# Kernel tuning notes

Measured on AMD Instinct MI355X. Metric: run time of the kernel, lower is better.

Reference implementation:

```python
import jax, jax.numpy as jnp
import numpy as np

# Layered-DAG regularization of the dynamic active_path graph.
H, N, BATCH, D, R = 6, 16, 32, 512, 64   # hop levels, nodes/level, batch, dim, low-rank
M = (H - 1) * N                           # nodes with weights (levels 1..H-1)
ETA_W = 0.015
LAM_C, LAM_R = 0.65, 0.35
THETA0 = 0.5
SPEC_MIN, SPEC_MAX = 0.3, 4.0
BETA1, BETA2, EPS = 0.9, 0.999, 1e-8
W_MAX = float(np.sqrt(D) * 2.0)
DW_CLIP = 5.0


def _spectral_norm(A1, B1):
    # largest singular value of W = A1 @ B1.T via power iteration using only low-rank products
    d = A1.shape[0]
    def body(_, u):
        w = A1 @ (B1.T @ (B1 @ (A1.T @ u)))  # (W W^T) u
        return w / (jnp.linalg.norm(w) + 1e-12)
    u0 = jnp.ones((d,), A1.dtype) / jnp.sqrt(jnp.asarray(d, A1.dtype))
    u = jax.lax.fori_loop(0, 20, body, u0)
    return jnp.linalg.norm(B1 @ (A1.T @ u))


def _update_node(A1, B1, mA, vA, mB, vB, Vin, T_local):
    # dual-signal (contrastive + retrograde) weight update, Adam step t=1, is_positive=True
    W = A1 @ B1.T                       # (D, D)
    Vw = Vin @ W.T                      # (BATCH, D) pre-activation (record.V_weighted)
    Vout = jnp.tanh(Vw)                 # record.V_out (tanh primitive)
    fprime = 1.0 - Vout ** 2            # primitive_derivative for tanh
    goodness = (Vout ** 2).sum(-1).mean()
    theta = THETA0 * ((Vin ** 2).sum(-1).mean() + 1e-9)   # goodness_scale_input=True
    delta = goodness - theta
    Vout_grad = (Vout * fprime * delta).mean(0)
    Vin_mean = Vin.mean(0)
    dW_c = jnp.outer(Vout_grad, Vin_mean)
    dW_r = jnp.outer(T_local.mean(0) * fprime.mean(0), Vin_mean)
    dW = LAM_C * dW_c + LAM_R * dW_r
    gnorm = jnp.linalg.norm(dW)
    dW = dW * jnp.where(gnorm > DW_CLIP, DW_CLIP / (gnorm + 1e-12), 1.0)
    gA = dW @ B1
    gB = dW.T @ A1
    mA_n = BETA1 * mA + (1 - BETA1) * gA
    vA_n = BETA2 * vA + (1 - BETA2) * gA ** 2
    A_new = A1 - ETA_W * (mA_n / (1 - BETA1)) / (jnp.sqrt(vA_n / (1 - BETA2)) + EPS)
    mB_n = BETA1 * mB + (1 - BETA1) * gB
    vB_n = BETA2 * vB + (1 - BETA2) * gB ** 2
    B_new = B1 - ETA_W * (mB_n / (1 - BETA1)) / (jnp.sqrt(vB_n / (1 - BETA2)) + EPS)
    return jnp.clip(A_new, -W_MAX, W_MAX), jnp.clip(B_new, -W_MAX, W_MAX)


def _forward(Y_hat, Y_star, V_edges, A, Bw, m_A, v_A, m_B, v_B):
    T_v = (Y_star - Y_hat) / jnp.sqrt(jnp.asarray(D, Y_hat.dtype))
    mse = jnp.mean((Y_star - Y_hat) ** 2)

    # proportional blame: per-edge mean-over-batch L2 norm of the contribution
    norms = jnp.linalg.norm(V_edges, axis=-1).mean(-1)           # (H-1, Ndst, Nsrc)
    w_blame = norms / (norms.sum(-1, keepdims=True) + 1e-9)

    spec = jax.vmap(jax.vmap(_spectral_norm))(A, Bw)             # (H-1, N)
    scale = jax.lax.stop_gradient(jnp.clip(spec, SPEC_MIN, SPEC_MAX))  # torch.tensor() detaches

    # retrograde flow in reverse topological (hop) order; output node = (level H-1, node 0)
    T_top = jnp.zeros((N, BATCH, D), Y_hat.dtype).at[0].set(T_v)

    def step(T_curr, xs):
        w_h, s_h = xs                                            # (Ndst,Nsrc), (Ndst,)
        tnorm = jnp.linalg.norm(T_curr, axis=-1).mean(-1)        # (Ndst,)
        edge_t = s_h[:, None] * w_h * tnorm[:, None]             # ||T_upstream|| per edge
        T_prev = jnp.einsum('j,ji,jbd->ibd', s_h, w_h, T_curr)   # blame-weighted scatter
        return T_prev, (T_prev, edge_t)

    _, (Ts, edge_t) = jax.lax.scan(step, T_top, (w_blame[::-1], scale[::-1]))
    T_all = jnp.concatenate([Ts[::-1], T_top[None]], axis=0)     # (H, N, BATCH, D), by level
    edge_tensions = edge_t[::-1]                                 # (H-1, Ndst, Nsrc)

    V_in = V_edges.sum(axis=2)                                   # inbox sum -> (H-1, N, BATCH, D)
    T_upd = T_all[1:]                                            # tensions at non-input nodes

    sh = (M, D, R)
    A_new, B_new = jax.vmap(_update_node)(
        A.reshape(sh), Bw.reshape(sh), m_A.reshape(sh), v_A.reshape(sh),
        m_B.reshape(sh), v_B.reshape(sh),
        V_in.reshape(M, BATCH, D), T_upd.reshape(M, BATCH, D))
    return (mse, edge_tensions,
            A_new.reshape(H - 1, N, D, R), B_new.reshape(H - 1, N, D, R), T_all)


def setup_inputs():
    key = jax.random.key(0)
    k = jax.random.split(key, 7)
    sd = 1.0 / np.sqrt(D)
    return {
        "Y_hat": jax.random.normal(k[0], (BATCH, D), jnp.float32),
        "Y_star": jax.random.normal(k[1], (BATCH, D), jnp.float32),
        "V_edges": jax.random.normal(k[2], (H - 1, N, N, BATCH, D), jnp.float32),
        "A": jax.random.normal(k[3], (H - 1, N, D, R), jnp.float32) * sd,
        "Bw": jax.random.normal(k[4], (H - 1, N, D, R), jnp.float32) * sd,
        "m_A": jnp.zeros((H - 1, N, D, R), jnp.float32),
        "v_A": jax.random.uniform(k[5], (H - 1, N, D, R), jnp.float32) * 1e-4,
        "m_B": jnp.zeros((H - 1, N, D, R), jnp.float32),
        "v_B": jax.random.uniform(k[6], (H - 1, N, D, R), jnp.float32) * 1e-4,
    }


def reference(Y_hat, Y_star, V_edges, A, Bw, m_A, v_A, m_B, v_B):
    return _forward(Y_hat, Y_star, V_edges, A, Bw, m_A, v_A, m_B, v_B)
```

## Files before the change

kernel.cpp:

```cpp
#include <hip/hip_runtime.h>
#include <math.h>

#define DEV static __device__ __forceinline__

constexpr int NB    = 16;
constexpr int BATCH = 32;
constexpr int DDIM  = 512;
constexpr int RK    = 64;
constexpr int LAY   = 5;
constexpr int MM    = 80;
constexpr int TLS   = NB * BATCH * DDIM;

constexpr float ETA_W   = 0.015f;
constexpr float LAM_C   = 0.65f, LAM_R = 0.35f;
constexpr float THETA0  = 0.5f;
constexpr float SPEC_MIN = 0.3f, SPEC_MAX = 4.0f;
constexpr float DW_CLIP = 5.0f;
constexpr float W_MAX   = 45.254833995939045f;
constexpr float RSQ_D   = 0.044194173824159216f;

constexpr int OUT_MSE  = 0;
constexpr int OUT_EDGE = 1;
constexpr int OUT_A    = 1281;
constexpr int OUT_B    = OUT_A + MM * DDIM * RK;
constexpr int OUT_T    = OUT_B + MM * DDIM * RK;

constexpr int SCR_GP   = 1284;
constexpr int SCR_VIN  = SCR_GP + 2621440;

constexpr int WS_NORMB  = 0;
constexpr int WS_TVN    = 40960;
constexpr int WS_TVM    = 41000;
constexpr int WS_COEF   = 41600;
constexpr int WS_SCALE  = 41700;
constexpr int WS_Y0P    = 41800;
constexpr int WS_VM     = 62300;
constexpr int WS_P      = 103300;
constexpr int WS_Q      = 108450;
constexpr int WS_GC     = 113600;

DEV float wave_reduce(float v) {
  #pragma unroll
  for (int o = 32; o > 0; o >>= 1) v += __shfl_down(v, o, 64);
  return v;
}

DEV float block_reduce_512(float v, float* sred) {
  v = wave_reduce(v);
  __syncthreads();
  if ((threadIdx.x & 63) == 0) sred[threadIdx.x >> 6] = v;
  __syncthreads();
  float s = 0.f;
  #pragma unroll
  for (int k = 0; k < 8; ++k) s += sred[k];
  return s;
}

DEV float bcast_lane(float v, int lane) {
  return __int_as_float(__builtin_amdgcn_readlane(__float_as_int(v), lane));
}

__global__ __launch_bounds__(256) void k_stage1(const float* __restrict__ V,
    const float* __restrict__ yh, const float* __restrict__ ys,
    const float* __restrict__ Aw, const float* __restrict__ Bww,
    float* __restrict__ out, float* __restrict__ ws) {
  __shared__ float smem[8448];
  int bid = blockIdx.x, t = threadIdx.x;
  if (bid < 2560) {
    float (*sbuf)[256] = (float(*)[256])smem;
    int b = bid & 31, j = (bid >> 5) & 15, hh = bid >> 9;
    const float* base = V + (size_t)(((hh*16 + j)*16)*32 + b) * 512;
    float ax = 0.f, ay = 0.f;
    #pragma unroll
    for (int i = 0; i < 16; ++i) {
      float2 vv = ((const float2*)(base + (size_t)i * 16384))[t];
      sbuf[i][t] = vv.x*vv.x + vv.y*vv.y;
      ax += vv.x; ay += vv.y;
    }
    float2 o; o.x = ax; o.y = ay;
    ((float2*)(out + SCR_VIN + (size_t)((hh*16 + j)*32 + b) * 512))[t] = o;
    __syncthreads();
    int w = t >> 6, lane = t & 63;
    #pragma unroll
    for (int k = 0; k < 4; ++k) {
      int i = w * 4 + k;
      float s = sbuf[i][lane] + sbuf[i][lane+64] + sbuf[i][lane+128] + sbuf[i][lane+192];
      s = wave_reduce(s);
      if (lane == 0)
        ws[WS_NORMB + (size_t)((hh*16 + j)*16 + i) * 32 + b] = sqrtf(s);
    }
  } else if (bid < 2592) {
    int b = bid - 2560;
    float2 a = ((const float2*)(yh + (size_t)b * 512))[t];
    float2 c = ((const float2*)(ys + (size_t)b * 512))[t];
    float d0 = c.x - a.x, d1 = c.y - a.y;
    float s = d0*d0 + d1*d1;
    s = wave_reduce(s);
    if ((t & 63) == 0) smem[t >> 6] = s;
    __syncthreads();
    if (t == 0)
      ws[WS_TVN + b] = sqrtf(smem[0]+smem[1]+smem[2]+smem[3]) * RSQ_D;
  } else if (bid == 2592) {
    float s = 0.f;
    for (int i = t; i < 4096; i += 256) {
      float4 a = ((const float4*)yh)[i], b = ((const float4*)ys)[i];
      float d0 = b.x-a.x, d1 = b.y-a.y, d2 = b.z-a.z, d3 = b.w-a.w;
      s += d0*d0 + d1*d1 + d2*d2 + d3*d3;
    }
    s = wave_reduce(s);
    if ((t & 63) == 0) smem[t >> 6] = s;
    __syncthreads();
    if (t == 0)
      out[OUT_MSE] = (smem[0]+smem[1]+smem[2]+smem[3]) * (1.f/16384.f);
  } else if (bid == 2593) {
    float s0 = 0.f, s1 = 0.f;
    #pragma unroll 4
    for (int b = 0; b < 32; ++b) {
      s0 += ys[b*512 + t]       - yh[b*512 + t];
      s1 += ys[b*512 + t + 256] - yh[b*512 + t + 256];
    }
    ws[WS_TVM + t]       = s0 * (RSQ_D / 32.f);
    ws[WS_TVM + t + 256] = s1 * (RSQ_D / 32.f);
  } else {
    float* tile = smem;
    float (*y0s)[64] = (float(*)[64])(smem + 8192);
    int bid0 = bid - 2594;
    int slice = bid0 & 3, side = (bid0 >> 2) & 1, m = bid0 >> 3;
    const float* src = (side ? Bww : Aw) + (size_t)m * 32768 + slice * 8192;
    #pragma unroll
    for (int k = 0; k < 8; ++k)
      ((float4*)tile)[t + k * 256] = ((const float4*)src)[t + k * 256];
    __syncthreads();
    {
      int r = t & 63, q = t >> 6;
      float s = 0.f;
      #pragma unroll 8
      for (int dd = q * 32; dd < q * 32 + 32; ++dd) s += tile[dd * 64 + r];
      y0s[q][r] = s;
    }
    __syncthreads();
    if (side == 0 && t < 64)
      ws[WS_Y0P + (m * 4 + slice) * 64 + t] = y0s[0][t] + y0s[1][t] + y0s[2][t] + y0s[3][t];
    float acc[4][4];
    #pragma unroll
    for (int i = 0; i < 4; ++i)
      #pragma unroll
      for (int k = 0; k < 4; ++k) acc[i][k] = 0.f;
    int r1 = (t >> 4) * 4, r2 = (t & 15) * 4;
    #pragma unroll 4
    for (int dd = 0; dd < 128; ++dd) {
      float4 a1 = *(const float4*)&tile[dd * 64 + r1];
      float4 a2 = *(const float4*)&tile[dd * 64 + r2];
      float av[4] = {a1.x, a1.y, a1.z, a1.w};
      float bv[4] = {a2.x, a2.y, a2.z, a2.w};
      #pragma unroll
      for (int i = 0; i < 4; ++i)
        #pragma unroll
        for (int k = 0; k < 4; ++k) acc[i][k] += av[i] * bv[k];
    }
    float* outp = out + SCR_GP + (size_t)((m * 2 + side) * 4 + slice) * 4096;
    #pragma unroll
    for (int i = 0; i < 4; ++i) {
      float4 v; v.x = acc[i][0]; v.y = acc[i][1]; v.z = acc[i][2]; v.w = acc[i][3];
      *(float4*)&outp[(r1 + i) * 64 + r2] = v;
    }
  }
}

__global__ __launch_bounds__(64, 1) void k_power(const float* __restrict__ out,
                                                 float* __restrict__ ws) {
  int m = blockIdx.x;
  int r = threadIdx.x;
  const float* gp = out + SCR_GP + (size_t)(m * 2 + 0) * 16384;
  const float* hp = out + SCR_GP + (size_t)(m * 2 + 1) * 16384;
  float Gc[64], Hc[64];
  #pragma unroll
  for (int c4 = 0; c4 < 16; ++c4) {
    const float* gb = gp + r * 64 + c4 * 4;
    float4 g0 = *(const float4*)(gb);
    float4 g1 = *(const float4*)(gb + 4096);
    float4 g2 = *(const float4*)(gb + 8192);
    float4 g3 = *(const float4*)(gb + 12288);
    Gc[c4*4+0] = g0.x+g1.x+g2.x+g3.x;
    Gc[c4*4+1] = g0.y+g1.y+g2.y+g3.y;
    Gc[c4*4+2] = g0.z+g1.z+g2.z+g3.z;
    Gc[c4*4+3] = g0.w+g1.w+g2.w+g3.w;
    const float* hb = hp + r * 64 + c4 * 4;
    float4 h0 = *(const float4*)(hb);
    float4 h1 = *(const float4*)(hb + 4096);
    float4 h2 = *(const float4*)(hb + 8192);
    float4 h3 = *(const float4*)(hb + 12288);
    Hc[c4*4+0] = h0.x+h1.x+h2.x+h3.x;
    Hc[c4*4+1] = h0.y+h1.y+h2.y+h3.y;
    Hc[c4*4+2] = h0.z+h1.z+h2.z+h3.z;
    Hc[c4*4+3] = h0.w+h1.w+h2.w+h3.w;
  }
  float y = (ws[WS_Y0P + (m*4+0)*64 + r] + ws[WS_Y0P + (m*4+1)*64 + r] +
             ws[WS_Y0P + (m*4+2)*64 + r] + ws[WS_Y0P + (m*4+3)*64 + r]) * RSQ_D;
  for (int it = 0; it < 20; ++it) {
    float z0 = 0.f, z1 = 0.f, z2 = 0.f, z3 = 0.f;
    #pragma unroll
    for (int c = 0; c < 16; ++c) {
      z0 = fmaf(Hc[c],      bcast_lane(y, c),      z0);
      z1 = fmaf(Hc[c + 16], bcast_lane(y, c + 16), z1);
      z2 = fmaf(Hc[c + 32], bcast_lane(y, c + 32), z2);
      z3 = fmaf(Hc[c + 48], bcast_lane(y, c + 48), z3);
    }
    float z = (z0 + z1) + (z2 + z3);
    float t0 = 0.f, t1 = 0.f, t2 = 0.f, t3 = 0.f;
    #pragma unroll
    for (int c = 0; c < 16; ++c) {
      t0 = fmaf(Gc[c],      bcast_lane(z, c),      t0);
      t1 = fmaf(Gc[c + 16], bcast_lane(z, c + 16), t1);
      t2 = fmaf(Gc[c + 32], bcast_lane(z, c + 32), t2);
      t3 = fmaf(Gc[c + 48], bcast_lane(z, c + 48), t3);
    }
    float tt = (t0 + t1) + (t2 + t3);
    float zt = z * tt;
    #pragma unroll
    for (int o = 32; o > 0; o >>= 1) zt += __shfl_xor(zt, o, 64);
    y = tt / (sqrtf(zt) + 1e-12f);
  }
  float z0 = 0.f, z1 = 0.f, z2 = 0.f, z3 = 0.f;
  #pragma unroll
  for (int c = 0; c < 16; ++c) {
    z0 = fmaf(Hc[c],      bcast_lane(y, c),      z0);
    z1 = fmaf(Hc[c + 16], bcast_lane(y, c + 16), z1);
    z2 = fmaf(Hc[c + 32], bcast_lane(y, c + 32), z2);
    z3 = fmaf(Hc[c + 48], bcast_lane(y, c + 48), z3);
  }
  float z = (z0 + z1) + (z2 + z3);
  float yz = y * z;
  #pragma unroll
  for (int o = 32; o > 0; o >>= 1) yz += __shfl_xor(yz, o, 64);
  if (r == 0)
    ws[WS_SCALE + m] = fminf(fmaxf(sqrtf(yz), SPEC_MIN), SPEC_MAX);
}

__global__ __launch_bounds__(256) void k_cc(float* __restrict__ ws,
                                            float* __restrict__ out) {
  __shared__ float C[5 * 256];
  __shared__ float coef[6 * 16];
  int t = threadIdx.x;
  int j = t >> 4;
  #pragma unroll
  for (int h = 0; h < 5; ++h) {
    const float* nb = ws + WS_NORMB + (size_t)(h * 256 + t) * 32;
    float n = 0.f;
    #pragma unroll 8
    for (int b = 0; b < 32; ++b) n += nb[b];
    n *= (1.f / 32.f);
    float s = n;
    s += __shfl_xor(s, 1, 64);
    s += __shfl_xor(s, 2, 64);
    s += __shfl_xor(s, 4, 64);
    s += __shfl_xor(s, 8, 64);
    C[h * 256 + t] = ws[WS_SCALE + h * 16 + j] * n / (s + 1e-9f);
  }
  if (t < 16) coef[5 * 16 + t] = (t == 0) ? 1.f : 0.f;
  __syncthreads();
  if (t < 16) {
    for (int h = 4; h >= 0; --h) {
      float s = 0.f;
      #pragma unroll
      for (int jj = 0; jj < 16; ++jj)
        s += C[h * 256 + jj * 16 + t] * coef[(h + 1) * 16 + jj];
      coef[h * 16 + t] = s;
    }
  }
  __syncthreads();
  float tvs = 0.f;
  #pragma unroll
  for (int b = 0; b < 32; ++b) tvs += ws[WS_TVN + b];
  float tvmean = tvs * (1.f / 32.f);
  #pragma unroll
  for (int h = 0; h < 5; ++h)
    out[OUT_EDGE + h * 256 + t] = C[h * 256 + t] * coef[(h + 1) * 16 + j] * tvmean;
  if (t < 96) ws[WS_COEF + t] = coef[t];
}

constexpr int MTP = 516;
constexpr int YVP = 36;

__global__ __launch_bounds__(512) void k_node(const float* __restrict__ Aw,
    const float* __restrict__ Bww, const float* out_all, float* __restrict__ ws) {
  __shared__ float MT[64 * MTP];
  __shared__ float R2[4096];
  __shared__ float gcol[512];
  __shared__ float sred[8];
  int m = blockIdx.x;
  int t = threadIdx.x;
  const float* A1  = Aw  + (size_t)m * 32768;
  const float* B1  = Bww + (size_t)m * 32768;
  const float* Vin = out_all + SCR_VIN + (size_t)m * 16384;
  int hh = m >> 4, j = m & 15;
  float coefval = ws[WS_COEF + (hh + 1) * 16 + j];

  auto stageT = [&](const float* src) {
    #pragma unroll
    for (int ch = 0; ch < 16; ++ch) {
      int g = ch * 2048 + t * 4;
      int d = g >> 6, r = g & 63;
      float4 v = *(const float4*)(src + g);
      MT[(r+0)*MTP + d] = v.x;
      MT[(r+1)*MTP + d] = v.y;
      MT[(r+2)*MTP + d] = v.z;
      MT[(r+3)*MTP + d] = v.w;
    }
  };

  stageT(B1);
  __syncthreads();

  {
    int rl = t & 31, bq = t >> 5;
    int b0 = bq * 2;
    float a00 = 0.f, a01 = 0.f, a10 = 0.f, a11 = 0.f;
    const float4* vp0 = (const float4*)(Vin + (size_t)b0 * 512);
    const float4* vp1 = (const float4*)(Vin + (size_t)(b0 + 1) * 512);
    #pragma unroll 4
    for (int d4 = 0; d4 < 128; ++d4) {
      float4 m0 = *(const float4*)&MT[rl * MTP + d4 * 4];
      float4 m1 = *(const float4*)&MT[(rl + 32) * MTP + d4 * 4];
      float4 v0 = vp0[d4];
      float4 v1 = vp1[d4];
      a00 += m0.x*v0.x + m0.y*v0.y + m0.z*v0.z + m0.w*v0.w;
      a01 += m0.x*v1.x + m0.y*v1.y + m0.z*v1.z + m0.w*v1.w;
      a10 += m1.x*v0.x + m1.y*v0.y + m1.z*v0.z + m1.w*v0.w;
      a11 += m1.x*v1.x + m1.y*v1.y + m1.z*v1.z + m1.w*v1.w;
    }
    R2[rl * YVP + b0]            = a00;
    R2[rl * YVP + b0 + 1]        = a01;
    R2[(rl + 32) * YVP + b0]     = a10;
    R2[(rl + 32) * YVP + b0 + 1] = a11;
  }
  __syncthreads();
  if (t < 64) {
    float s = 0.f;
    #pragma unroll 8
    for (int b = 0; b < 32; ++b) s += R2[t * YVP + b];
    ws[WS_P + m * 64 + t] = s * (1.f / 32.f);
  }
  float tmean, ssin, ssvm;
  {
    int d = t;
    float sv = 0.f, sq = 0.f;
    #pragma unroll 4
    for (int b = 0; b < 32; ++b) {
      float v = Vin[b * 512 + d];
      sv += v; sq += v * v;
    }
    float vmean = sv * (1.f / 32.f);
    tmean = coefval * ws[WS_TVM + d];
    ws[WS_VM + m * 512 + d] = vmean;
    ssin = block_reduce_512(sq, sred) * (1.f / 32.f);
    ssvm = block_reduce_512(vmean * vmean, sred);
  }
  __syncthreads();
  stageT(A1);
  __syncthreads();
  float gs = 0.f;
  float vga[4] = {0.f, 0.f, 0.f, 0.f}, fpa[4] = {0.f, 0.f, 0.f, 0.f};
  {
    int d4 = t >> 2, bg = t & 3;
    float acc[4][8];
    #pragma unroll
    for (int i = 0; i < 4; ++i)
      #pragma unroll
      for (int k = 0; k < 8; ++k) acc[i][k] = 0.f;
    #pragma unroll 2
    for (int rr = 0; rr < 64; ++rr) {
      float4 at = *(const float4*)&MT[rr * MTP + d4 * 4];
      float4 ya = *(const float4*)&R2[rr * YVP + bg * 8];
      float4 yb = *(const float4*)&R2[rr * YVP + bg * 8 + 4];
      float av[4] = {at.x, at.y, at.z, at.w};
      float yv[8] = {ya.x, ya.y, ya.z, ya.w, yb.x, yb.y, yb.z, yb.w};
      #pragma unroll
      for (int i = 0; i < 4; ++i)
        #pragma unroll
        for (int k = 0; k < 8; ++k) acc[i][k] += av[i] * yv[k];
    }
    #pragma unroll
    for (int i = 0; i < 4; ++i)
      #pragma unroll
      for (int k = 0; k < 8; ++k) {
        float vw = acc[i][k];
        float x = fminf(fmaxf(vw * 2.f, -40.f), 40.f);
        float e = __expf(x);
        float vo = (e - 1.f) / (e + 1.f);
        float fp = 1.f - vo * vo;
        gs += vo * vo;
        vga[i] += vo * fp;
        fpa[i] += fp;
      }
  }
  __syncthreads();
  {
    int d4 = t >> 2, bg = t & 3;
    #pragma unroll
    for (int i = 0; i < 4; ++i) {
      R2[bg * 512 + d4 * 4 + i] = vga[i];
      R2[2048 + bg * 512 + d4 * 4 + i] = fpa[i];
    }
  }
  float goodness = block_reduce_512(gs, sred) * (1.f / 32.f);
  float delta = goodness - THETA0 * (ssin + 1e-9f);
  {
    int d = t;
    float vg = R2[d] + R2[512 + d] + R2[1024 + d] + R2[1536 + d];
    float fp = R2[2048 + d] + R2[2048 + 512 + d] + R2[2048 + 1024 + d] + R2[2048 + 1536 + d];
    float g = LAM_C * delta * vg * (1.f / 32.f) + LAM_R * tmean * (fp * (1.f / 32.f));
    float gn2 = block_reduce_512(g * g, sred);
    float gnorm = sqrtf(gn2) * sqrtf(ssvm);
    float clipf = gnorm > DW_CLIP ? DW_CLIP / (gnorm + 1e-12f) : 1.f;
    float gcv = g * clipf;
    ws[WS_GC + m * 512 + d] = gcv;
    gcol[d] = gcv;
  }
  __syncthreads();
  {
    int r = t & 63, dq = t >> 6;
    float s = 0.f;
    #pragma unroll
    for (int k = 0; k < 16; ++k) {
      int d = dq * 64 + k * 4;
      float4 at = *(const float4*)&MT[r * MTP + d];
      float4 gv = *(const float4*)&gcol[d];
      s += at.x*gv.x + at.y*gv.y + at.z*gv.z + at.w*gv.w;
    }
    R2[dq * 64 + r] = s;
  }
  __syncthreads();
  if (t < 64) {
    float s = 0.f;
    #pragma unroll
    for (int p8 = 0; p8 < 8; ++p8) s += R2[p8 * 64 + t];
    ws[WS_Q + m * 64 + t] = s;
  }
}

constexpr int TW_BLOCKS = 1536;
constexpr int AD_HALF4  = 655360;

__global__ __launch_bounds__(256) void k_final(const float* __restrict__ yh,
    const float* __restrict__ ys,
    const float* __restrict__ Aw, const float* __restrict__ Bww,
    const float* __restrict__ mA, const float* __restrict__ vA,
    const float* __restrict__ mB, const float* __restrict__ vB,
    const float* __restrict__ ws, float* __restrict__ out) {
  int bid = blockIdx.x, t = threadIdx.x;
  if (bid < TW_BLOCKS) {
    int g0 = (bid * 256 + t) * 4;
    int li = g0 >> 14;
    int bd = g0 & 16383;
    float4 a = *(const float4*)(yh + bd);
    float4 b = *(const float4*)(ys + bd);
    float cf = ws[WS_COEF + li] * RSQ_D;
    out[OUT_T + g0 + 0] = cf * (b.x - a.x);
    out[OUT_T + g0 + 1] = cf * (b.y - a.y);
    out[OUT_T + g0 + 2] = cf * (b.z - a.z);
    out[OUT_T + g0 + 3] = cf * (b.w - a.w);
    return;
  }
  int idx = (bid - TW_BLOCKS) * 256 + t;
  bool isB = idx >= AD_HALF4;
  int e = (isB ? idx - AD_HALF4 : idx) * 4;
  int m = e >> 15;
  int rem = e & 32767;
  int d = rem >> 6;
  int r = rem & 63;
  float4 g4;
  const float *w0, *m0, *v0;
  int obase;
  if (!isB) {
    float gc = ws[WS_GC + m * 512 + d];
    float4 p = *(const float4*)&ws[WS_P + m * 64 + r];
    g4.x = gc * p.x; g4.y = gc * p.y; g4.z = gc * p.z; g4.w = gc * p.w;
    w0 = Aw; m0 = mA; v0 = vA; obase = OUT_A;
  } else {
    float vm = ws[WS_VM + m * 512 + d];
    float4 q = *(const float4*)&ws[WS_Q + m * 64 + r];
    g4.x = vm * q.x; g4.y = vm * q.y; g4.z = vm * q.z; g4.w = vm * q.w;
    w0 = Bww; m0 = mB; v0 = vB; obase = OUT_B;
  }
  float4 a4 = *(const float4*)&w0[e];
  float4 mm4 = *(const float4*)&m0[e];
  float4 vv4 = *(const float4*)&v0[e];
  float ga[4] = {g4.x, g4.y, g4.z, g4.w};
  float aa[4] = {a4.x, a4.y, a4.z, a4.w};
  float ma[4] = {mm4.x, mm4.y, mm4.z, mm4.w};
  float va[4] = {vv4.x, vv4.y, vv4.z, vv4.w};
  #pragma unroll
  for (int i = 0; i < 4; ++i) {
    float g = ga[i];
    float mn = 0.9f * ma[i] + 0.1f * g;
    float vn = 0.999f * va[i] + 0.001f * g * g;
    float u = aa[i] - ETA_W * (mn * 10.f) / (sqrtf(vn * 1000.f) + 1e-8f);
    u = fminf(fmaxf(u, -W_MAX), W_MAX);
    out[obase + e + i] = u;
  }
}

extern "C" void kernel_launch(void* const* d_in, const int* in_sizes, int n_in,
                              void* d_out, int out_size, void* d_ws, size_t ws_size,
                              hipStream_t stream) {
  (void)in_sizes; (void)n_in; (void)out_size; (void)ws_size;
  const float* Yh = (const float*)d_in[0];
  const float* Ys = (const float*)d_in[1];
  const float* V  = (const float*)d_in[2];
  const float* Aw = (const float*)d_in[3];
  const float* Bw = (const float*)d_in[4];
  const float* mA = (const float*)d_in[5];
  const float* vA = (const float*)d_in[6];
  const float* mB = (const float*)d_in[7];
  const float* vB = (const float*)d_in[8];
  float* out = (float*)d_out;
  float* ws  = (float*)d_ws;

  k_stage1<<<2594 + 640, 256, 0, stream>>>(V, Yh, Ys, Aw, Bw, out, ws);
  k_power<<<80, 64, 0, stream>>>(out, ws);
  k_cc<<<1, 256, 0, stream>>>(ws, out);
  k_node<<<80, 512, 0, stream>>>(Aw, Bw, out, ws);
  k_final<<<TW_BLOCKS + 2 * (AD_HALF4 / 256), 256, 0, stream>>>(
      Yh, Ys, Aw, Bw, mA, vA, mB, vB, ws, out);
}
```

Before: 115.1 us.

## Fuse power iteration and coefficient kernels via last-block atomic counter; widen stage1 loads

Merges k_power and k_cc into one kernel. The last block to finish, found through an atomic counter in the workspace, computes the edge coefficients, which removes one kernel launch and its dependency gap. Stage1 now reads V with float4 loads split across two thread groups and combines the partial sums through shared memory. The cost is a serialized tail: a single 64-thread block does the coefficient work that used 256 threads before. The design also relies on the counter reset in stage1 and on threadfence ordering between blocks.

After: 131.4 us. 14.2% more time.

```diff
diff --git a/kernel.cpp b/kernel.cpp
--- a/kernel.cpp
+++ b/kernel.cpp
@@ -33,6 +33,7 @@
 constexpr int WS_TVM    = 41000;
 constexpr int WS_COEF   = 41600;
 constexpr int WS_SCALE  = 41700;
+constexpr int WS_CTR    = 41784;
 constexpr int WS_Y0P    = 41800;
 constexpr int WS_VM     = 62300;
 constexpr int WS_P      = 103300;
@@ -67,24 +68,35 @@
   __shared__ float smem[8448];
   int bid = blockIdx.x, t = threadIdx.x;
   if (bid < 2560) {
-    float (*sbuf)[256] = (float(*)[256])smem;
+    float* nbuf = smem;
+    float* vbuf = smem + 2048;
     int b = bid & 31, j = (bid >> 5) & 15, hh = bid >> 9;
     const float* base = V + (size_t)(((hh*16 + j)*16)*32 + b) * 512;
-    float ax = 0.f, ay = 0.f;
-    #pragma unroll
-    for (int i = 0; i < 16; ++i) {
-      float2 vv = ((const float2*)(base + (size_t)i * 16384))[t];
-      sbuf[i][t] = vv.x*vv.x + vv.y*vv.y;
-      ax += vv.x; ay += vv.y;
-    }
-    float2 o; o.x = ax; o.y = ay;
-    ((float2*)(out + SCR_VIN + (size_t)((hh*16 + j)*32 + b) * 512))[t] = o;
+    int g = t >> 7, u = t & 127;
+    float vx = 0.f, vy = 0.f, vz = 0.f, vw = 0.f;
+    #pragma unroll
+    for (int io = 0; io < 8; ++io) {
+      int i = io * 2 + g;
+      float4 v = ((const float4*)(base + (size_t)i * 16384))[u];
+      nbuf[i * 128 + u] = v.x*v.x + v.y*v.y + v.z*v.z + v.w*v.w;
+      vx += v.x; vy += v.y; vz += v.z; vw += v.w;
+    }
+    vbuf[g * 512 + u * 4 + 0] = vx;
+    vbuf[g * 512 + u * 4 + 1] = vy;
+    vbuf[g * 512 + u * 4 + 2] = vz;
+    vbuf[g * 512 + u * 4 + 3] = vw;
     __syncthreads();
+    {
+      float2 o;
+      o.x = vbuf[2 * t]     + vbuf[512 + 2 * t];
+      o.y = vbuf[2 * t + 1] + vbuf[512 + 2 * t + 1];
+      ((float2*)(out + SCR_VIN + (size_t)((hh*16 + j)*32 + b) * 512))[t] = o;
+    }
     int w = t >> 6, lane = t & 63;
     #pragma unroll
     for (int k = 0; k < 4; ++k) {
       int i = w * 4 + k;
-      float s = sbuf[i][lane] + sbuf[i][lane+64] + sbuf[i][lane+128] + sbuf[i][lane+192];
+      float s = nbuf[i * 128 + lane] + nbuf[i * 128 + lane + 64];
       s = wave_reduce(s);
       if (lane == 0)
         ws[WS_NORMB + (size_t)((hh*16 + j)*16 + i) * 32 + b] = sqrtf(s);
@@ -113,6 +125,7 @@
     if (t == 0)
       out[OUT_MSE] = (smem[0]+smem[1]+smem[2]+smem[3]) * (1.f/16384.f);
   } else if (bid == 2593) {
+    if (t == 0) *((int*)(ws + WS_CTR)) = 0;
     float s0 = 0.f, s1 = 0.f;
     #pragma unroll 4
     for (int b = 0; b < 32; ++b) {
@@ -167,37 +180,63 @@
   }
 }
 
-__global__ __launch_bounds__(64, 1) void k_power(const float* __restrict__ out,
-                                                 float* __restrict__ ws) {
+__global__ __launch_bounds__(64, 1) void k_pcc(const float* __restrict__ out,
+                                               float* __restrict__ ws) {
+  __shared__ float C[5 * 256];
+  __shared__ float coefs[6 * 16];
   int m = blockIdx.x;
   int r = threadIdx.x;
-  const float* gp = out + SCR_GP + (size_t)(m * 2 + 0) * 16384;
-  const float* hp = out + SCR_GP + (size_t)(m * 2 + 1) * 16384;
-  float Gc[64], Hc[64];
-  #pragma unroll
-  for (int c4 = 0; c4 < 16; ++c4) {
-    const float* gb = gp + r * 64 + c4 * 4;
-    float4 g0 = *(const float4*)(gb);
-    float4 g1 = *(const float4*)(gb + 4096);
-    float4 g2 = *(const float4*)(gb + 8192);
-    float4 g3 = *(const float4*)(gb + 12288);
-    Gc[c4*4+0] = g0.x+g1.x+g2.x+g3.x;
-    Gc[c4*4+1] = g0.y+g1.y+g2.y+g3.y;
-    Gc[c4*4+2] = g0.z+g1.z+g2.z+g3.z;
-    Gc[c4*4+3] = g0.w+g1.w+g2.w+g3.w;
-    const float* hb = hp + r * 64 + c4 * 4;
-    float4 h0 = *(const float4*)(hb);
-    float4 h1 = *(const float4*)(hb + 4096);
-    float4 h2 = *(const float4*)(hb + 8192);
-    float4 h3 = *(const float4*)(hb + 12288);
-    Hc[c4*4+0] = h0.x+h1.x+h2.x+h3.x;
-    Hc[c4*4+1] = h0.y+h1.y+h2.y+h3.y;
-    Hc[c4*4+2] = h0.z+h1.z+h2.z+h3.z;
-    Hc[c4*4+3] = h0.w+h1.w+h2.w+h3.w;
-  }
-  float y = (ws[WS_Y0P + (m*4+0)*64 + r] + ws[WS_Y0P + (m*4+1)*64 + r] +
-             ws[WS_Y0P + (m*4+2)*64 + r] + ws[WS_Y0P + (m*4+3)*64 + r]) * RSQ_D;
-  for (int it = 0; it < 20; ++it) {
+  {
+    const float* gp = out + SCR_GP + (size_t)(m * 2 + 0) * 16384;
+    const float* hp = out + SCR_GP + (size_t)(m * 2 + 1) * 16384;
+    float Gc[64], Hc[64];
+    #pragma unroll
+    for (int c4 = 0; c4 < 16; ++c4) {
+      const float* gb = gp + r * 64 + c4 * 4;
+      float4 g0 = *(const float4*)(gb);
+      float4 g1 = *(const float4*)(gb + 4096);
+      float4 g2 = *(const float4*)(gb + 8192);
+      float4 g3 = *(const float4*)(gb + 12288);
+      Gc[c4*4+0] = g0.x+g1.x+g2.x+g3.x;
+      Gc[c4*4+1] = g0.y+g1.y+g2.y+g3.y;
+      Gc[c4*4+2] = g0.z+g1.z+g2.z+g3.z;
+      Gc[c4*4+3] = g0.w+g1.w+g2.w+g3.w;
+      const float* hb = hp + r * 64 + c4 * 4;
+      float4 h0 = *(const float4*)(hb);
+      float4 h1 = *(const float4*)(hb + 4096);
+      float4 h2 = *(const float4*)(hb + 8192);
+      float4 h3 = *(const float4*)(hb + 12288);
+      Hc[c4*4+0] = h0.x+h1.x+h2.x+h3.x;
+      Hc[c4*4+1] = h0.y+h1.y+h2.y+h3.y;
+      Hc[c4*4+2] = h0.z+h1.z+h2.z+h3.z;
+      Hc[c4*4+3] = h0.w+h1.w+h2.w+h3.w;
+    }
+    float y = (ws[WS_Y0P + (m*4+0)*64 + r] + ws[WS_Y0P + (m*4+1)*64 + r] +
+               ws[WS_Y0P + (m*4+2)*64 + r] + ws[WS_Y0P + (m*4+3)*64 + r]) * RSQ_D;
+    for (int it = 0; it < 20; ++it) {
+      float z0 = 0.f, z1 = 0.f, z2 = 0.f, z3 = 0.f;
+      #pragma unroll
+      for (int c = 0; c < 16; ++c) {
+        z0 = fmaf(Hc[c],      bcast_lane(y, c),      z0);
+        z1 = fmaf(Hc[c + 16], bcast_lane(y, c + 16), z1);
+        z2 = fmaf(Hc[c + 32], bcast_lane(y, c + 32), z2);
+        z3 = fmaf(Hc[c + 48], bcast_lane(y, c + 48), z3);
+      }
+      float z = (z0 + z1) + (z2 + z3);
+      float t0 = 0.f, t1 = 0.f, t2 = 0.f, t3 = 0.f;
+      #pragma unroll
+      for (int c = 0; c < 16; ++c) {
+        t0 = fmaf(Gc[c],      bcast_lane(z, c),      t0);
+        t1 = fmaf(Gc[c + 16], bcast_lane(z, c + 16), t1);
+        t2 = fmaf(Gc[c + 32], bcast_lane(z, c + 32), t2);
+        t3 = fmaf(Gc[c + 48], bcast_lane(z, c + 48), t3);
+      }
+      float tt = (t0 + t1) + (t2 + t3);
+      float zt = z * tt;
+      #pragma unroll
+      for (int o = 32; o > 0; o >>= 1) zt += __shfl_xor(zt, o, 64);
+      y = tt / (sqrtf(zt) + 1e-12f);
+    }
     float z0 = 0.f, z1 = 0.f, z2 = 0.f, z3 = 0.f;
     #pragma unroll
     for (int c = 0; c < 16; ++c) {
@@ -207,65 +246,48 @@
       z3 = fmaf(Hc[c + 48], bcast_lane(y, c + 48), z3);
     }
     float z = (z0 + z1) + (z2 + z3);
-    float t0 = 0.f, t1 = 0.f, t2 = 0.f, t3 = 0.f;
-    #pragma unroll
-    for (int c = 0; c < 16; ++c) {
-      t0 = fmaf(Gc[c],      bcast_lane(z, c),      t0);
-      t1 = fmaf(Gc[c + 16], bcast_lane(z, c + 16), t1);
-      t2 = fmaf(Gc[c + 32], bcast_lane(z, c + 32), t2);
-      t3 = fmaf(Gc[c + 48], bcast_lane(z, c + 48), t3);
-    }
-    float tt = (t0 + t1) + (t2 + t3);
-    float zt = z * tt;
-    #pragma unroll
-    for (int o = 32; o > 0; o >>= 1) zt += __shfl_xor(zt, o, 64);
-    y = tt / (sqrtf(zt) + 1e-12f);
-  }
-  float z0 = 0.f, z1 = 0.f, z2 = 0.f, z3 = 0.f;
+    float yz = y * z;
+    #pragma unroll
+    for (int o = 32; o > 0; o >>= 1) yz += __shfl_xor(yz, o, 64);
+    if (r == 0)
+      ws[WS_SCALE + m] = fminf(fmaxf(sqrtf(yz), SPEC_MIN), SPEC_MAX);
+  }
+  __threadfence();
+  int old = 0;
+  if (r == 0) old = atomicAdd((int*)(ws + WS_CTR), 1);
+  old = __shfl(old, 0, 64);
+  if (old != MM - 1) return;
+  __threadfence();
+  float* wout = (float*)0;
+  (void)wout;
   #pragma unroll
-  for (int c = 0; c < 16; ++c) {
-    z0 = fmaf(Hc[c],      bcast_lane(y, c),      z0);
-    z1 = fmaf(Hc[c + 16], bcast_lane(y, c + 16), z1);
-    z2 = fmaf(Hc[c + 32], bcast_lane(y, c + 32), z2);
-    z3 = fmaf(Hc[c + 48], bcast_lane(y, c + 48), z3);
-  }
-  float z = (z0 + z1) + (z2 + z3);
-  float yz = y * z;
-  #pragma unroll
-  for (int o = 32; o > 0; o >>= 1) yz += __shfl_xor(yz, o, 64);
-  if (r == 0)
-    ws[WS_SCALE + m] = fminf(fmaxf(sqrtf(yz), SPEC_MIN), SPEC_MAX);
-}
-
-__global__ __launch_bounds__(256) void k_cc(float* __restrict__ ws,
-                                            float* __restrict__ out) {
-  __shared__ float C[5 * 256];
-  __shared__ float coef[6 * 16];
-  int t = threadIdx.x;
-  int j = t >> 4;
-  #pragma unroll
-  for (int h = 0; h < 5; ++h) {
-    const float* nb = ws + WS_NORMB + (size_t)(h * 256 + t) * 32;
-    float n = 0.f;
-    #pragma unroll 8
-    for (int b = 0; b < 32; ++b) n += nb[b];
-    n *= (1.f / 32.f);
-    float s = n;
-    s += __shfl_xor(s, 1, 64);
-    s += __shfl_xor(s, 2, 64);
-    s += __shfl_xor(s, 4, 64);
-    s += __shfl_xor(s, 8, 64);
-    C[h * 256 + t] = ws[WS_SCALE + h * 16 + j] * n / (s + 1e-9f);
-  }
-  if (t < 16) coef[5 * 16 + t] = (t == 0) ? 1.f : 0.f;
-  __syncthreads();
-  if (t < 16) {
+  for (int k = 0; k < 4; ++k) {
+    int tt = k * 64 + r;
+    int j = tt >> 4;
+    #pragma unroll
+    for (int h = 0; h < 5; ++h) {
+      const float* nb = ws + WS_NORMB + (size_t)(h * 256 + tt) * 32;
+      float n = 0.f;
+      #pragma unroll 8
+      for (int b = 0; b < 32; ++b) n += nb[b];
+      n *= (1.f / 32.f);
+      float s = n;
+      s += __shfl_xor(s, 1, 64);
+      s += __shfl_xor(s, 2, 64);
+      s += __shfl_xor(s, 4, 64);
+      s += __shfl_xor(s, 8, 64);
+      C[h * 256 + tt] = ws[WS_SCALE + h * 16 + j] * n / (s + 1e-9f);
+    }
+  }
+  if (r < 16) coefs[5 * 16 + r] = (r == 0) ? 1.f : 0.f;
+  __syncthreads();
+  if (r < 16) {
     for (int h = 4; h >= 0; --h) {
       float s = 0.f;
       #pragma unroll
       for (int jj = 0; jj < 16; ++jj)
-        s += C[h * 256 + jj * 16 + t] * coef[(h + 1) * 16 + jj];
-      coef[h * 16 + t] = s;
+        s += C[h * 256 + jj * 16 + r] * coefs[(h + 1) * 16 + jj];
+      coefs[h * 16 + r] = s;
     }
   }
   __syncthreads();
@@ -273,10 +295,15 @@
   #pragma unroll
   for (int b = 0; b < 32; ++b) tvs += ws[WS_TVN + b];
   float tvmean = tvs * (1.f / 32.f);
+  float* outw = (float*)out;
   #pragma unroll
-  for (int h = 0; h < 5; ++h)
-    out[OUT_EDGE + h * 256 + t] = C[h * 256 + t] * coef[(h + 1) * 16 + j] * tvmean;
-  if (t < 96) ws[WS_COEF + t] = coef[t];
+  for (int k = 0; k < 4; ++k) {
+    int tt = k * 64 + r;
+    #pragma unroll
+    for (int h = 0; h < 5; ++h)
+      outw[OUT_EDGE + h * 256 + tt] = C[h * 256 + tt] * coefs[(h + 1) * 16 + (tt >> 4)] * tvmean;
+  }
+  for (int idx = r; idx < 96; idx += 64) ws[WS_COEF + idx] = coefs[idx];
 }
 
 constexpr int MTP = 516;
@@ -518,8 +545,7 @@
   float* ws  = (float*)d_ws;
 
   k_stage1<<<2594 + 640, 256, 0, stream>>>(V, Yh, Ys, Aw, Bw, out, ws);
-  k_power<<<80, 64, 0, stream>>>(out, ws);
-  k_cc<<<1, 256, 0, stream>>>(ws, out);
+  k_pcc<<<80, 64, 0, stream>>>(out, ws);
   k_node<<<80, 512, 0, stream>>>(Aw, Bw, out, ws);
   k_final<<<TW_BLOCKS + 2 * (AD_HALF4 / 256), 256, 0, stream>>>(
       Yh, Ys, Aw, Bw, mA, vA, mB, vB, ws, out);
```
